# Performance work log

Measured on AMD Instinct MI355X. Metric: run time of the kernel, lower is better.

## Reference

```python
import jax, jax.numpy as jnp
import numpy as np

T, B, IN_DIM = 512, 256, 256
H1, H = 512, 256          # fc hidden, GRU hidden
OUT_DIM = 18


def setup_inputs() -> dict:
    key = jax.random.key(0)
    ks = jax.random.split(key, 14)
    s = 0.05
    return {
        "x":      jax.random.normal(ks[0], (T, B, IN_DIM), dtype=jnp.float32),
        # fc1: Linear(IN_DIM,H1)+ReLU, Linear(H1,H)+ReLU
        "W_fc1a": jax.random.normal(ks[1], (H1, IN_DIM), dtype=jnp.float32) * s,
        "b_fc1a": jax.random.normal(ks[2], (H1,), dtype=jnp.float32) * s,
        "W_fc1b": jax.random.normal(ks[3], (H, H1), dtype=jnp.float32) * s,
        "b_fc1b": jax.random.normal(ks[4], (H,), dtype=jnp.float32) * s,
        # GRUCell(H, H): weights ordered [r, z, n] like torch
        "W_ih":   jax.random.normal(ks[5], (3 * H, H), dtype=jnp.float32) * s,
        "b_ih":   jax.random.normal(ks[6], (3 * H,), dtype=jnp.float32) * s,
        "W_hh":   jax.random.normal(ks[7], (3 * H, H), dtype=jnp.float32) * s,
        "b_hh":   jax.random.normal(ks[8], (3 * H,), dtype=jnp.float32) * s,
        # fc2: Linear(H,H1)+ReLU, Linear(H1,OUT_DIM)
        "W_fc2a": jax.random.normal(ks[9], (H1, H), dtype=jnp.float32) * s,
        "b_fc2a": jax.random.normal(ks[10], (H1,), dtype=jnp.float32) * s,
        "W_fc2b": jax.random.normal(ks[11], (OUT_DIM, H1), dtype=jnp.float32) * s,
        "b_fc2b": jax.random.normal(ks[12], (OUT_DIM,), dtype=jnp.float32) * s,
    }


def reference(x, W_fc1a, b_fc1a, W_fc1b, b_fc1b,
              W_ih, b_ih, W_hh, b_hh,
              W_fc2a, b_fc2a, W_fc2b, b_fc2b):
    batch = x.shape[1]
    h0 = jnp.zeros((batch, W_hh.shape[1]), dtype=x.dtype)

    def step(h, xt):
        # fc1 MLP
        a = jax.nn.relu(xt @ W_fc1a.T + b_fc1a)
        a = jax.nn.relu(a @ W_fc1b.T + b_fc1b)
        # GRUCell (torch gate order r, z, n)
        gi = a @ W_ih.T + b_ih            # [B, 3H]
        gh = h @ W_hh.T + b_hh            # [B, 3H]
        i_r, i_z, i_n = jnp.split(gi, 3, axis=-1)
        h_r, h_z, h_n = jnp.split(gh, 3, axis=-1)
        r = jax.nn.sigmoid(i_r + h_r)
        z = jax.nn.sigmoid(i_z + h_z)
        n = jnp.tanh(i_n + r * h_n)
        h_new = (1.0 - z) * n + z * h
        # fc2 head
        q = jax.nn.relu(h_new @ W_fc2a.T + b_fc2a) @ W_fc2b.T + b_fc2b
        return h_new, q

    _, qs = jax.lax.scan(step, h0, x)     # qs: [T, B, OUT_DIM]
    return qs
```

## Files before the change

### kernel.cpp

```cpp
#include <hip/hip_runtime.h>
#include <hip/hip_fp16.h>
#include <cstdio>

typedef unsigned short u16;
typedef __attribute__((ext_vector_type(8))) _Float16 f16x8;
typedef __attribute__((ext_vector_type(4))) float fv4;

#define TT 512
#define BB 256

__device__ __forceinline__ float us2f(u16 u) {
    union { u16 u; _Float16 h; } c; c.u = u; return (float)c.h;
}
__device__ __forceinline__ u16 f2us(float f) {
    union { u16 u; _Float16 h; } c; c.h = (_Float16)f; return c.u;
}

__device__ __forceinline__ void gl_lds16(const u16* g, u16* l) {
    __builtin_amdgcn_global_load_lds(
        (const __attribute__((address_space(1))) void*)g,
        (__attribute__((address_space(3))) void*)l, 16, 0, 0);
}

__global__ void cvt_f32_f16(const float* __restrict__ s, u16* __restrict__ d, int n) {
    long stride = (long)gridDim.x * blockDim.x * 8;
    for (long i = ((long)blockIdx.x * blockDim.x + threadIdx.x) * 8; i < n; i += stride) {
        f16x8 o;
#pragma unroll
        for (int j = 0; j < 8; ++j) o[j] = (_Float16)s[i + j];
        *(f16x8*)(d + i) = o;
    }
}

__global__ void bias_fold(const float* __restrict__ bih, const float* __restrict__ bhh,
                          float* __restrict__ bsum) {
    int i = blockIdx.x * blockDim.x + threadIdx.x;
    if (i < 768) bsum[i] = bih[i] + (i < 512 ? bhh[i] : 0.f);
}

__global__ void pack_whh(const float* __restrict__ W, u16* __restrict__ Wp) {
    int t = blockIdx.x * blockDim.x + threadIdx.x;
    int l = t & 63;
    int kt = (t >> 6) & 7;
    int jt = t >> 9;
    int j = jt * 16 + (l & 15);
    int k = kt * 32 + (l >> 4) * 8;
    f16x8 o;
#pragma unroll
    for (int i = 0; i < 8; ++i) o[i] = (_Float16)W[j * 256 + k + i];
    *(f16x8*)(Wp + (size_t)t * 8) = o;
}

__global__ void pack_w2b(const float* __restrict__ W, u16* __restrict__ Wp) {
    int t = blockIdx.x * blockDim.x + threadIdx.x;
    int l = t & 63;
    int kt = (t >> 6) & 15;
    int nt = t >> 10;
    int n = nt * 16 + (l & 15);
    int k = kt * 32 + (l >> 4) * 8;
    f16x8 o;
#pragma unroll
    for (int i = 0; i < 8; ++i)
        o[i] = (n < 18) ? (_Float16)W[n * 512 + k + i] : (_Float16)0.f;
    *(f16x8*)(Wp + (size_t)t * 8) = o;
}

__global__ __launch_bounds__(256) void gemm_bt(
    const u16* __restrict__ A, const u16* __restrict__ B,
    const float* __restrict__ bias, u16* __restrict__ C,
    int N, int K, int act)
{
    __shared__ u16 Ash[4096] __attribute__((aligned(16)));
    __shared__ u16 Bsh[4096] __attribute__((aligned(16)));
    const int tid = threadIdx.x;
    const int l = tid & 63, w = tid >> 6;
    const long m0 = (long)blockIdx.y * 128;
    const int n0 = blockIdx.x * 128;
    const int r = tid >> 2, c8 = (tid & 3) * 8;
    const u16* gA0 = A + (m0 + r) * K + c8;
    const u16* gA1 = A + (m0 + 64 + r) * K + c8;
    const u16* gB0 = B + (long)(n0 + r) * K + c8;
    const u16* gB1 = B + (long)(n0 + 64 + r) * K + c8;
    const int mb = (w >> 1) * 64, nb = (w & 1) * 64;
    const int mrow = l & 15, colq = (l >> 4) * 8;
    fv4 acc[4][4] = {};
    for (int k0 = 0; k0 < K; k0 += 32) {
        gl_lds16(gA0 + k0, &Ash[tid * 8]);
        gl_lds16(gA1 + k0, &Ash[2048 + tid * 8]);
        gl_lds16(gB0 + k0, &Bsh[tid * 8]);
        gl_lds16(gB1 + k0, &Bsh[2048 + tid * 8]);
        __syncthreads();
        f16x8 af[4], bf[4];
#pragma unroll
        for (int i = 0; i < 4; ++i)
            af[i] = *(const f16x8*)&Ash[(mb + i * 16 + mrow) * 32 + colq];
#pragma unroll
        for (int i = 0; i < 4; ++i)
            bf[i] = *(const f16x8*)&Bsh[(nb + i * 16 + mrow) * 32 + colq];
#pragma unroll
        for (int mt = 0; mt < 4; ++mt)
#pragma unroll
            for (int nt = 0; nt < 4; ++nt)
                acc[mt][nt] = __builtin_amdgcn_mfma_f32_16x16x32_f16(
                    af[mt], bf[nt], acc[mt][nt], 0, 0, 0);
        __syncthreads();
    }
    float bv[4];
#pragma unroll
    for (int nt = 0; nt < 4; ++nt) bv[nt] = bias[n0 + nb + nt * 16 + mrow];
    const int rq = (l >> 4) * 4;
#pragma unroll
    for (int mt = 0; mt < 4; ++mt)
#pragma unroll
        for (int nt = 0; nt < 4; ++nt)
#pragma unroll
            for (int i = 0; i < 4; ++i) {
                float v = acc[mt][nt][i] + bv[nt];
                if (act) v = fmaxf(v, 0.f);
                C[(m0 + mb + mt * 16 + rq + i) * (long)N + (n0 + nb + nt * 16 + mrow)] = f2us(v);
            }
}

__global__ __launch_bounds__(256) void gemm_gi(
    const u16* __restrict__ A, const u16* __restrict__ B,
    const float* __restrict__ bias, u16* __restrict__ GIp)
{
    __shared__ u16 Ash[4096] __attribute__((aligned(16)));
    __shared__ u16 Bsh[4096] __attribute__((aligned(16)));
    const int tid = threadIdx.x;
    const int l = tid & 63, w = tid >> 6;
    const long m0 = (long)blockIdx.y * 128;
    const int n0 = blockIdx.x * 128;
    const int r = tid >> 2, c8 = (tid & 3) * 8;
    const u16* gA0 = A + (m0 + r) * 256 + c8;
    const u16* gA1 = A + (m0 + 64 + r) * 256 + c8;
    const u16* gB0 = B + (long)(n0 + r) * 256 + c8;
    const u16* gB1 = B + (long)(n0 + 64 + r) * 256 + c8;
    const int mb = (w >> 1) * 64, nb = (w & 1) * 64;
    const int mrow = l & 15, colq = (l >> 4) * 8;
    fv4 acc[4][4] = {};
    for (int k0 = 0; k0 < 256; k0 += 32) {
        gl_lds16(gA0 + k0, &Ash[tid * 8]);
        gl_lds16(gA1 + k0, &Ash[2048 + tid * 8]);
        gl_lds16(gB0 + k0, &Bsh[tid * 8]);
        gl_lds16(gB1 + k0, &Bsh[2048 + tid * 8]);
        __syncthreads();
        f16x8 af[4], bf[4];
#pragma unroll
        for (int i = 0; i < 4; ++i)
            af[i] = *(const f16x8*)&Ash[(mb + i * 16 + mrow) * 32 + colq];
#pragma unroll
        for (int i = 0; i < 4; ++i)
            bf[i] = *(const f16x8*)&Bsh[(nb + i * 16 + mrow) * 32 + colq];
#pragma unroll
        for (int mt = 0; mt < 4; ++mt)
#pragma unroll
            for (int nt = 0; nt < 4; ++nt)
                acc[mt][nt] = __builtin_amdgcn_mfma_f32_16x16x32_f16(
                    af[mt], bf[nt], acc[mt][nt], 0, 0, 0);
        __syncthreads();
    }
    float bv[4];
#pragma unroll
    for (int nt = 0; nt < 4; ++nt) bv[nt] = bias[n0 + nb + nt * 16 + mrow];
    const int rq = (l >> 4) * 4;
#pragma unroll
    for (int mt = 0; mt < 4; ++mt)
#pragma unroll
        for (int nt = 0; nt < 4; ++nt)
#pragma unroll
            for (int i = 0; i < 4; ++i) {
                float v = acc[mt][nt][i] + bv[nt];
                int m = (int)(m0 + mb + mt * 16 + rq + i);
                int n = n0 + nb + nt * 16 + mrow;
                int t  = m >> 8, b = m & 255;
                int blk = b >> 4, rb = b & 15, q = rb >> 2, i2 = rb & 3;
                int g = n >> 8, c = n & 255, w2 = c >> 5, s = (c >> 4) & 1, cl = c & 15;
                size_t idx = ((((size_t)t * 16 + blk) * 8 + w2) * 64 + (q * 16 + cl)) * 24
                             + (g * 2 + s) * 4 + i2;
                GIp[idx] = f2us(v);
            }
}

__global__ __launch_bounds__(512, 2) void gru_seq4(
    const u16* __restrict__ Wp, const u16* __restrict__ GIp,
    const float* __restrict__ bhh, u16* __restrict__ Hout)
{
    __shared__ u16 h_sh[2][4096] __attribute__((aligned(16)));
    __shared__ u16 Wl[24576] __attribute__((aligned(16)));
    const int tid = threadIdx.x;
    const int l = tid & 63, w = tid >> 6;
    const int blk = blockIdx.x;
    const int bg = blk * 16;
    const int col = l & 15, quad = l >> 4;

    for (int i = tid; i < 4096; i += 512) h_sh[0][i] = 0;
    for (int idx = tid; idx < 3072; idx += 512)
        *(f16x8*)&Wl[(size_t)idx * 8] =
            *(const f16x8*)&Wp[(((size_t)(idx >> 6) * 8 + 7) * 64 + (idx & 63)) * 8];

    int jts[6];
#pragma unroll
    for (int g = 0; g < 3; ++g)
#pragma unroll
        for (int s = 0; s < 2; ++s) jts[g * 2 + s] = g * 16 + 2 * w + s;

    f16x8 wf[6][7];
#pragma unroll
    for (int u = 0; u < 6; ++u)
#pragma unroll
        for (int kt = 0; kt < 7; ++kt)
            wf[u][kt] = *(const f16x8*)&Wp[(((size_t)jts[u] * 8 + kt) * 64 + l) * 8];

    float hbn[2] = { bhh[512 + 32 * w + col], bhh[512 + 32 * w + 16 + col] };

    const u16* gbase = GIp + ((size_t)(blk * 8 + w) * 64 + l) * 24;
    f16x8 gcur[3], gnxt[3];
#pragma unroll
    for (int j = 0; j < 3; ++j) gcur[j] = *(const f16x8*)(gbase + j * 8);

    float hold[2][4] = {};
    u16* hout_base = Hout + ((size_t)(bg + quad * 4) * 256) + 32 * w + col;
    __syncthreads();

    for (int t = 0; t < TT; ++t) {
        const int rd = t & 1, wr = (t + 1) & 1;
        const u16* gn = gbase + (size_t)(t < TT - 1 ? t + 1 : t) * 196608;
#pragma unroll
        for (int j = 0; j < 3; ++j) gnxt[j] = *(const f16x8*)(gn + j * 8);

        fv4 acc[6] = {};
#pragma unroll
        for (int kt = 0; kt < 7; ++kt) {
            f16x8 a = *(const f16x8*)&h_sh[rd][(kt * 64 + l) * 8];
#pragma unroll
            for (int u = 0; u < 6; ++u)
                acc[u] = __builtin_amdgcn_mfma_f32_16x16x32_f16(a, wf[u][kt], acc[u], 0, 0, 0);
        }
        {
            f16x8 a = *(const f16x8*)&h_sh[rd][(7 * 64 + l) * 8];
#pragma unroll
            for (int u = 0; u < 6; ++u) {
                f16x8 bw = *(const f16x8*)&Wl[(size_t)(jts[u] * 64 + l) * 8];
                acc[u] = __builtin_amdgcn_mfma_f32_16x16x32_f16(a, bw, acc[u], 0, 0, 0);
            }
        }
        u16* hp = hout_base + (size_t)t * 65536;
#pragma unroll
        for (int s = 0; s < 2; ++s) {
            const int q2 = s * 2 + (col >> 3);
#pragma unroll
            for (int i = 0; i < 4; ++i) {
                float pr  = (float)gcur[0][s * 4 + i] + acc[0 + s][i];
                float pz  = (float)gcur[1][s * 4 + i] + acc[2 + s][i];
                float h_n = acc[4 + s][i] + hbn[s];
                float rg = __builtin_amdgcn_rcpf(1.f + __expf(-pr));
                float zg = __builtin_amdgcn_rcpf(1.f + __expf(-pz));
                float pre = (float)gcur[2][s * 4 + i] + rg * h_n;
                float ea = __expf(-2.f * fabsf(pre));
                float th = (1.f - ea) * __builtin_amdgcn_rcpf(1.f + ea);
                float ng = (pre >= 0.f) ? th : -th;
                float hn = (1.f - zg) * ng + zg * hold[s][i];
                hold[s][i] = hn;
                u16 hu = f2us(hn);
                h_sh[wr][(w * 64 + q2 * 16 + quad * 4 + i) * 8 + (col & 7)] = hu;
                hp[(size_t)i * 256 + s * 16] = hu;
            }
        }
#pragma unroll
        for (int j = 0; j < 3; ++j) gcur[j] = gnxt[j];
        __syncthreads();
    }
}

__global__ __launch_bounds__(256) void head_gemm(
    const u16* __restrict__ Q1, const u16* __restrict__ W2p,
    const float* __restrict__ b2, float* __restrict__ out)
{
    __shared__ u16 Ash[4096] __attribute__((aligned(16)));
    __shared__ u16 Bsh[16384] __attribute__((aligned(16)));
    const int tid = threadIdx.x;
    const int l = tid & 63, w = tid >> 6;
    const long m0 = (long)blockIdx.x * 128;
    const int col = l & 15, quad = l >> 4, colq = quad * 8;
    for (int i = tid * 8; i < 16384; i += 2048)
        *(f16x8*)&Bsh[i] = *(const f16x8*)&W2p[i];
    const int r = tid >> 2, c8 = (tid & 3) * 8;
    const u16* gA0 = Q1 + (m0 + r) * 512 + c8;
    const u16* gA1 = Q1 + (m0 + 64 + r) * 512 + c8;
    fv4 acc[2][2] = {};
    for (int k0 = 0; k0 < 512; k0 += 32) {
        gl_lds16(gA0 + k0, &Ash[tid * 8]);
        gl_lds16(gA1 + k0, &Ash[2048 + tid * 8]);
        __syncthreads();
        const int kt = k0 >> 5;
        f16x8 af[2], bf[2];
#pragma unroll
        for (int mt = 0; mt < 2; ++mt)
            af[mt] = *(const f16x8*)&Ash[(w * 32 + mt * 16 + col) * 32 + colq];
#pragma unroll
        for (int nt = 0; nt < 2; ++nt)
            bf[nt] = *(const f16x8*)&Bsh[((nt * 16 + kt) * 64 + l) * 8];
#pragma unroll
        for (int mt = 0; mt < 2; ++mt)
#pragma unroll
            for (int nt = 0; nt < 2; ++nt)
                acc[mt][nt] = __builtin_amdgcn_mfma_f32_16x16x32_f16(
                    af[mt], bf[nt], acc[mt][nt], 0, 0, 0);
        __syncthreads();
    }
    const int rq = quad * 4;
#pragma unroll
    for (int nt = 0; nt < 2; ++nt) {
        int c = nt * 16 + col;
        if (c < 18) {
            float bias = b2[c];
#pragma unroll
            for (int mt = 0; mt < 2; ++mt)
#pragma unroll
                for (int i = 0; i < 4; ++i)
                    out[(m0 + w * 32 + mt * 16 + rq + i) * 18 + c] = acc[mt][nt][i] + bias;
        }
    }
}

extern "C" void kernel_launch(void* const* d_in, const int* in_sizes, int n_in,
                              void* d_out, int out_size, void* d_ws, size_t ws_size,
                              hipStream_t stream) {
    const float* x   = (const float*)d_in[0];
    const float* W1a = (const float*)d_in[1];
    const float* b1a = (const float*)d_in[2];
    const float* W1b = (const float*)d_in[3];
    const float* b1b = (const float*)d_in[4];
    const float* Wih = (const float*)d_in[5];
    const float* bih = (const float*)d_in[6];
    const float* Whh = (const float*)d_in[7];
    const float* bhh = (const float*)d_in[8];
    const float* W2a = (const float*)d_in[9];
    const float* b2a = (const float*)d_in[10];
    const float* W2b = (const float*)d_in[11];
    const float* b2b = (const float*)d_in[12];

    char* ws = (char*)d_ws;
    u16* R    = (u16*)ws;
    u16* A2b  = (u16*)(ws + 201326592);
    u16* XH   = (u16*)(ws + 268435456);
    float* bsum = (float*)(ws + 268435456 + 67108864 - 4096);
    u16* W1ah = (u16*)(ws + 335544320);
    u16* W1bh = (u16*)(ws + 335806464);
    u16* Wihh = (u16*)(ws + 336068608);
    u16* W2ah = (u16*)(ws + 336461824);
    u16* Wpk  = (u16*)(ws + 336723968);
    u16* W2p  = (u16*)(ws + 337117184);
    if (ws_size < 337149952) {
        fprintf(stderr, "kernel_launch: ws too small (%zu < 337149952)\n", ws_size);
    }

    cvt_f32_f16<<<dim3(2048), dim3(256), 0, stream>>>(x, XH, 33554432);
    cvt_f32_f16<<<dim3(64), dim3(256), 0, stream>>>(W1a, W1ah, 131072);
    cvt_f32_f16<<<dim3(64), dim3(256), 0, stream>>>(W1b, W1bh, 131072);
    cvt_f32_f16<<<dim3(96), dim3(256), 0, stream>>>(Wih, Wihh, 196608);
    cvt_f32_f16<<<dim3(64), dim3(256), 0, stream>>>(W2a, W2ah, 131072);
    pack_whh<<<dim3(96), dim3(256), 0, stream>>>(Whh, Wpk);
    pack_w2b<<<dim3(8), dim3(256), 0, stream>>>(W2b, W2p);

    gemm_bt<<<dim3(4, 1024), dim3(256), 0, stream>>>(XH, W1ah, b1a, R,   512, 256, 1);
    bias_fold<<<dim3(3), dim3(256), 0, stream>>>(bih, bhh, bsum);
    gemm_bt<<<dim3(2, 1024), dim3(256), 0, stream>>>(R,  W1bh, b1b, A2b, 256, 512, 1);
    gemm_gi<<<dim3(6, 1024), dim3(256), 0, stream>>>(A2b, Wihh, bsum, R);
    gru_seq4<<<dim3(16), dim3(512), 0, stream>>>(Wpk, R, bhh, XH);
    gemm_bt<<<dim3(4, 1024), dim3(256), 0, stream>>>(XH, W2ah, b2a, R, 512, 256, 1);
    head_gemm<<<dim3(1024), dim3(256), 0, stream>>>(R, W2p, b2b, (float*)d_out);
}
```

Baseline: 1.468 ms.

## Store GRU hidden states in packed MFMA layout and add matching head GEMM

The GRU kernel now writes each step's hidden state as one coalesced 16-byte copy of the packed LDS tile, one step late, instead of scattered 2-byte stores per element. A new fc2a GEMM reads that packed fragment layout directly as its A operand, with no LDS staging for A. Two of the eight K-tiles of W_hh now live in LDS instead of one, and an empty asm pins the remaining weight fragments in registers, to cut register pressure and spills. The cost is more LDS per block and an extra LDS read each step for the hidden-state copy.

```diff
diff --git a/kernel.cpp b/kernel.cpp
--- a/kernel.cpp
+++ b/kernel.cpp
@@ -182,22 +182,23 @@
             }
 }
 
-__global__ __launch_bounds__(512, 2) void gru_seq4(
+__global__ __launch_bounds__(512, 2) void gru_seq5(
     const u16* __restrict__ Wp, const u16* __restrict__ GIp,
-    const float* __restrict__ bhh, u16* __restrict__ Hout)
+    const float* __restrict__ bhh, u16* __restrict__ Hp)
 {
     __shared__ u16 h_sh[2][4096] __attribute__((aligned(16)));
-    __shared__ u16 Wl[24576] __attribute__((aligned(16)));
+    __shared__ u16 Wl[49152] __attribute__((aligned(16)));
     const int tid = threadIdx.x;
     const int l = tid & 63, w = tid >> 6;
     const int blk = blockIdx.x;
-    const int bg = blk * 16;
     const int col = l & 15, quad = l >> 4;
 
     for (int i = tid; i < 4096; i += 512) h_sh[0][i] = 0;
-    for (int idx = tid; idx < 3072; idx += 512)
+    for (int idx = tid; idx < 6144; idx += 512) {
+        int kt6 = idx / 3072, rem = idx % 3072;
         *(f16x8*)&Wl[(size_t)idx * 8] =
-            *(const f16x8*)&Wp[(((size_t)(idx >> 6) * 8 + 7) * 64 + (idx & 63)) * 8];
+            *(const f16x8*)&Wp[(((size_t)(rem >> 6) * 8 + 6 + kt6) * 64 + (rem & 63)) * 8];
+    }
 
     int jts[6];
 #pragma unroll
@@ -205,12 +206,17 @@
 #pragma unroll
         for (int s = 0; s < 2; ++s) jts[g * 2 + s] = g * 16 + 2 * w + s;
 
-    f16x8 wf[6][7];
+    f16x8 wf[6][6];
 #pragma unroll
     for (int u = 0; u < 6; ++u)
 #pragma unroll
-        for (int kt = 0; kt < 7; ++kt)
+        for (int kt = 0; kt < 6; ++kt)
             wf[u][kt] = *(const f16x8*)&Wp[(((size_t)jts[u] * 8 + kt) * 64 + l) * 8];
+#pragma unroll
+    for (int u = 0; u < 6; ++u)
+#pragma unroll
+        for (int kt = 0; kt < 6; ++kt)
+            asm volatile("" : "+v"(wf[u][kt]));
 
     float hbn[2] = { bhh[512 + 32 * w + col], bhh[512 + 32 * w + 16 + col] };
 
@@ -220,32 +226,36 @@
     for (int j = 0; j < 3; ++j) gcur[j] = *(const f16x8*)(gbase + j * 8);
 
     float hold[2][4] = {};
-    u16* hout_base = Hout + ((size_t)(bg + quad * 4) * 256) + 32 * w + col;
+    u16* hp_base = Hp + (size_t)blk * 4096 + tid * 8;
     __syncthreads();
 
     for (int t = 0; t < TT; ++t) {
         const int rd = t & 1, wr = (t + 1) & 1;
+        if (t) {
+            f16x8 hv = *(const f16x8*)&h_sh[rd][tid * 8];
+            *(f16x8*)(hp_base + (size_t)(t - 1) * 65536) = hv;
+        }
         const u16* gn = gbase + (size_t)(t < TT - 1 ? t + 1 : t) * 196608;
 #pragma unroll
         for (int j = 0; j < 3; ++j) gnxt[j] = *(const f16x8*)(gn + j * 8);
 
         fv4 acc[6] = {};
 #pragma unroll
-        for (int kt = 0; kt < 7; ++kt) {
+        for (int kt = 0; kt < 6; ++kt) {
             f16x8 a = *(const f16x8*)&h_sh[rd][(kt * 64 + l) * 8];
 #pragma unroll
             for (int u = 0; u < 6; ++u)
                 acc[u] = __builtin_amdgcn_mfma_f32_16x16x32_f16(a, wf[u][kt], acc[u], 0, 0, 0);
         }
-        {
-            f16x8 a = *(const f16x8*)&h_sh[rd][(7 * 64 + l) * 8];
+#pragma unroll
+        for (int kt6 = 0; kt6 < 2; ++kt6) {
+            f16x8 a = *(const f16x8*)&h_sh[rd][((6 + kt6) * 64 + l) * 8];
 #pragma unroll
             for (int u = 0; u < 6; ++u) {
-                f16x8 bw = *(const f16x8*)&Wl[(size_t)(jts[u] * 64 + l) * 8];
+                f16x8 bw = *(const f16x8*)&Wl[((size_t)(kt6 * 48 + jts[u]) * 64 + l) * 8];
                 acc[u] = __builtin_amdgcn_mfma_f32_16x16x32_f16(a, bw, acc[u], 0, 0, 0);
             }
         }
-        u16* hp = hout_base + (size_t)t * 65536;
 #pragma unroll
         for (int s = 0; s < 2; ++s) {
             const int q2 = s * 2 + (col >> 3);
@@ -262,15 +272,70 @@
                 float ng = (pre >= 0.f) ? th : -th;
                 float hn = (1.f - zg) * ng + zg * hold[s][i];
                 hold[s][i] = hn;
-                u16 hu = f2us(hn);
-                h_sh[wr][(w * 64 + q2 * 16 + quad * 4 + i) * 8 + (col & 7)] = hu;
-                hp[(size_t)i * 256 + s * 16] = hu;
+                h_sh[wr][(w * 64 + q2 * 16 + quad * 4 + i) * 8 + (col & 7)] = f2us(hn);
             }
         }
 #pragma unroll
         for (int j = 0; j < 3; ++j) gcur[j] = gnxt[j];
         __syncthreads();
     }
+    {
+        f16x8 hv = *(const f16x8*)&h_sh[0][tid * 8];
+        *(f16x8*)(hp_base + (size_t)511 * 65536) = hv;
+    }
+}
+
+__global__ __launch_bounds__(256) void gemm_hp(
+    const u16* __restrict__ Hp, const u16* __restrict__ B,
+    const float* __restrict__ bias, u16* __restrict__ C)
+{
+    __shared__ u16 Bsh[4096] __attribute__((aligned(16)));
+    const int tid = threadIdx.x;
+    const int l = tid & 63, w = tid >> 6;
+    const long m0 = (long)blockIdx.y * 128;
+    const int n0 = blockIdx.x * 128;
+    const int r = tid >> 2, c8 = (tid & 3) * 8;
+    const u16* gB0 = B + (long)(n0 + r) * 256 + c8;
+    const u16* gB1 = B + (long)(n0 + 64 + r) * 256 + c8;
+    const int mb = (w >> 1) * 64, nb = (w & 1) * 64;
+    const int mrow = l & 15, colq = (l >> 4) * 8;
+    const int t = (int)(m0 >> 8), half = ((int)m0 >> 7) & 1;
+    const u16* aBase = Hp + ((size_t)t * 16 + half * 8 + (mb >> 4)) * 4096 + (size_t)l * 8;
+    fv4 acc[4][4] = {};
+    for (int k0 = 0; k0 < 256; k0 += 32) {
+        gl_lds16(gB0 + k0, &Bsh[tid * 8]);
+        gl_lds16(gB1 + k0, &Bsh[2048 + tid * 8]);
+        const int kt = k0 >> 5;
+        f16x8 af[4];
+#pragma unroll
+        for (int i = 0; i < 4; ++i)
+            af[i] = *(const f16x8*)(aBase + (size_t)i * 4096 + kt * 512);
+        __syncthreads();
+        f16x8 bf[4];
+#pragma unroll
+        for (int i = 0; i < 4; ++i)
+            bf[i] = *(const f16x8*)&Bsh[(nb + i * 16 + mrow) * 32 + colq];
+#pragma unroll
+        for (int mt = 0; mt < 4; ++mt)
+#pragma unroll
+            for (int nt = 0; nt < 4; ++nt)
+                acc[mt][nt] = __builtin_amdgcn_mfma_f32_16x16x32_f16(
+                    af[mt], bf[nt], acc[mt][nt], 0, 0, 0);
+        __syncthreads();
+    }
+    float bv[4];
+#pragma unroll
+    for (int nt = 0; nt < 4; ++nt) bv[nt] = bias[n0 + nb + nt * 16 + mrow];
+    const int rq = (l >> 4) * 4;
+#pragma unroll
+    for (int mt = 0; mt < 4; ++mt)
+#pragma unroll
+        for (int nt = 0; nt < 4; ++nt)
+#pragma unroll
+            for (int i = 0; i < 4; ++i) {
+                float v = fmaxf(acc[mt][nt][i] + bv[nt], 0.f);
+                C[(m0 + mb + mt * 16 + rq + i) * 512L + (n0 + nb + nt * 16 + mrow)] = f2us(v);
+            }
 }
 
 __global__ __launch_bounds__(256) void head_gemm(
@@ -368,7 +433,7 @@
     bias_fold<<<dim3(3), dim3(256), 0, stream>>>(bih, bhh, bsum);
     gemm_bt<<<dim3(2, 1024), dim3(256), 0, stream>>>(R,  W1bh, b1b, A2b, 256, 512, 1);
     gemm_gi<<<dim3(6, 1024), dim3(256), 0, stream>>>(A2b, Wihh, bsum, R);
-    gru_seq4<<<dim3(16), dim3(512), 0, stream>>>(Wpk, R, bhh, XH);
-    gemm_bt<<<dim3(4, 1024), dim3(256), 0, stream>>>(XH, W2ah, b2a, R, 512, 256, 1);
+    gru_seq5<<<dim3(16), dim3(512), 0, stream>>>(Wpk, R, bhh, XH);
+    gemm_hp<<<dim3(4, 1024), dim3(256), 0, stream>>>(XH, W2ah, b2a, R);
     head_gemm<<<dim3(1024), dim3(256), 0, stream>>>(R, W2p, b2b, (float*)d_out);
 }
```

Result: slower. 1.569 ms (+6.9%).
